# Optimization experiments

Measured on AMD Instinct MI355X. Metric: run time of the kernel, lower is better.

## Reference

```python
import jax, jax.numpy as jnp
import numpy as np

ND_WEIGHT = 1.0
NUM_CLASS = 1000
B, D = 16384, 2048


def setup_inputs() -> dict:
    key = jax.random.key(0)
    k1, k2, k3, k4 = jax.random.split(key, 4)
    s_emb = jax.random.normal(k1, (B, D), dtype=jnp.float32)
    t_emb = jax.random.normal(k2, (B, D), dtype=jnp.float32)
    T_EMB = jax.random.normal(k3, (NUM_CLASS, D), dtype=jnp.float32)
    labels = jax.random.randint(k4, (B,), 0, NUM_CLASS, dtype=jnp.int64)
    return {"s_emb": s_emb, "t_emb": t_emb, "T_EMB": T_EMB, "labels": labels}


def reference(s_emb, t_emb, T_EMB, labels):
    # Gather per-sample class centers: [B, D]
    centers = T_EMB[labels]
    # Unit-normalize each center (L2 along feature dim)
    e_c = centers / jnp.linalg.norm(centers, axis=-1, keepdims=True)
    # Per-sample max of student/teacher embedding norms: [B]
    s_norm = jnp.linalg.norm(s_emb, axis=-1)
    t_norm = jnp.linalg.norm(t_emb, axis=-1)
    max_norm = jnp.maximum(s_norm, t_norm)
    # 1 - <s, e_c> / max_norm, summed then averaged, scaled by nd_weight
    dots = jnp.sum(s_emb * e_c, axis=-1)
    loss_sum = jnp.sum(1.0 - dots / max_norm)
    return loss_sum * ND_WEIGHT / s_emb.shape[0]
```

## Files before the change

kernel.cpp:

```cpp
#include <hip/hip_runtime.h>


#define NROWS 16384
#define DDIM  2048
#define BLK   256

__global__ __launch_bounds__(BLK) void dnl_row_kernel(
    const float* __restrict__ s_emb,
    const float* __restrict__ t_emb,
    const float* __restrict__ T_EMB,
    const int*   __restrict__ labels,
    float*       __restrict__ partial)
{
    const int row = blockIdx.x;
    const int tid = threadIdx.x;
    const int label = labels[row];

    const float4* s4 = (const float4*)(s_emb + (size_t)row   * DDIM);
    const float4* t4 = (const float4*)(t_emb + (size_t)row   * DDIM);
    const float4* c4 = (const float4*)(T_EMB + (size_t)label * DDIM);

    float ss = 0.f, tt = 0.f, sc = 0.f, cc = 0.f;
    #pragma unroll
    for (int it = 0; it < 2; ++it) {
        const int k = tid + it * BLK;
        const float4 s = s4[k];
        const float4 t = t4[k];
        const float4 c = c4[k];
        ss += s.x*s.x + s.y*s.y + s.z*s.z + s.w*s.w;
        tt += t.x*t.x + t.y*t.y + t.z*t.z + t.w*t.w;
        sc += s.x*c.x + s.y*c.y + s.z*c.z + s.w*c.w;
        cc += c.x*c.x + c.y*c.y + c.z*c.z + c.w*c.w;
    }

    #pragma unroll
    for (int off = 32; off > 0; off >>= 1) {
        ss += __shfl_down(ss, off, 64);
        tt += __shfl_down(tt, off, 64);
        sc += __shfl_down(sc, off, 64);
        cc += __shfl_down(cc, off, 64);
    }

    __shared__ float red[4][4];
    const int wave = tid >> 6;
    const int lane = tid & 63;
    if (lane == 0) {
        red[wave][0] = ss; red[wave][1] = tt;
        red[wave][2] = sc; red[wave][3] = cc;
    }
    __syncthreads();

    if (tid == 0) {
        float SS = 0.f, TT = 0.f, SC = 0.f, CC = 0.f;
        #pragma unroll
        for (int w = 0; w < 4; ++w) {
            SS += red[w][0]; TT += red[w][1];
            SC += red[w][2]; CC += red[w][3];
        }
        const float max_norm = fmaxf(sqrtf(SS), sqrtf(TT));
        partial[row] = 1.0f - SC / (sqrtf(CC) * max_norm);
    }
}

__global__ __launch_bounds__(BLK) void dnl_row_kernel_atomic(
    const float* __restrict__ s_emb,
    const float* __restrict__ t_emb,
    const float* __restrict__ T_EMB,
    const int*   __restrict__ labels,
    float*       __restrict__ out)
{
    const int row = blockIdx.x;
    const int tid = threadIdx.x;
    const int label = labels[row];

    const float4* s4 = (const float4*)(s_emb + (size_t)row   * DDIM);
    const float4* t4 = (const float4*)(t_emb + (size_t)row   * DDIM);
    const float4* c4 = (const float4*)(T_EMB + (size_t)label * DDIM);

    float ss = 0.f, tt = 0.f, sc = 0.f, cc = 0.f;
    #pragma unroll
    for (int it = 0; it < 2; ++it) {
        const int k = tid + it * BLK;
        const float4 s = s4[k];
        const float4 t = t4[k];
        const float4 c = c4[k];
        ss += s.x*s.x + s.y*s.y + s.z*s.z + s.w*s.w;
        tt += t.x*t.x + t.y*t.y + t.z*t.z + t.w*t.w;
        sc += s.x*c.x + s.y*c.y + s.z*c.z + s.w*c.w;
        cc += c.x*c.x + c.y*c.y + c.z*c.z + c.w*c.w;
    }
    #pragma unroll
    for (int off = 32; off > 0; off >>= 1) {
        ss += __shfl_down(ss, off, 64);
        tt += __shfl_down(tt, off, 64);
        sc += __shfl_down(sc, off, 64);
        cc += __shfl_down(cc, off, 64);
    }
    __shared__ float red[4][4];
    const int wave = tid >> 6;
    const int lane = tid & 63;
    if (lane == 0) {
        red[wave][0] = ss; red[wave][1] = tt;
        red[wave][2] = sc; red[wave][3] = cc;
    }
    __syncthreads();
    if (tid == 0) {
        float SS = 0.f, TT = 0.f, SC = 0.f, CC = 0.f;
        #pragma unroll
        for (int w = 0; w < 4; ++w) {
            SS += red[w][0]; TT += red[w][1];
            SC += red[w][2]; CC += red[w][3];
        }
        const float max_norm = fmaxf(sqrtf(SS), sqrtf(TT));
        const float contrib = 1.0f - SC / (sqrtf(CC) * max_norm);
        atomicAdd(out, contrib * (1.0f / (float)NROWS));
    }
}

__global__ __launch_bounds__(BLK) void dnl_reduce_kernel(
    const float* __restrict__ partial,
    float*       __restrict__ out)
{
    const int tid = threadIdx.x;
    float sum = 0.f;
    for (int i = tid; i < NROWS; i += BLK) sum += partial[i];

    #pragma unroll
    for (int off = 32; off > 0; off >>= 1)
        sum += __shfl_down(sum, off, 64);

    __shared__ float red[4];
    if ((tid & 63) == 0) red[tid >> 6] = sum;
    __syncthreads();
    if (tid == 0)
        out[0] = (red[0] + red[1] + red[2] + red[3]) * (1.0f / (float)NROWS);
}

extern "C" void kernel_launch(void* const* d_in, const int* in_sizes, int n_in,
                              void* d_out, int out_size, void* d_ws, size_t ws_size,
                              hipStream_t stream) {
    const float* s_emb  = (const float*)d_in[0];
    const float* t_emb  = (const float*)d_in[1];
    const float* T_EMB  = (const float*)d_in[2];
    const int*   labels = (const int*)d_in[3];
    float* out = (float*)d_out;

    if (ws_size >= (size_t)NROWS * sizeof(float)) {
        float* partial = (float*)d_ws;
        dnl_row_kernel<<<NROWS, BLK, 0, stream>>>(s_emb, t_emb, T_EMB, labels, partial);
        dnl_reduce_kernel<<<1, BLK, 0, stream>>>(partial, out);
    } else {
        hipMemsetAsync(d_out, 0, sizeof(float), stream);
        dnl_row_kernel_atomic<<<NROWS, BLK, 0, stream>>>(s_emb, t_emb, T_EMB, labels, out);
    }
}
```

Measured before the change: 298.9 us.

## Process one row per wavefront in a persistent grid with per-wave accumulation

Replaces the one-block-per-row launch (16384 blocks) with a persistent grid of 1024 blocks where each 64-lane wavefront handles whole rows in a strided loop. Rows are reduced with xor shuffles only, so the shared-memory stage and __syncthreads go away, and each wave keeps a running sum plus a prefetched next label. The final reduction reads 4096 per-wave partials with float4 loads instead of 16384 per-row values. Each wave now issues 24 float4 loads per row, which gives more memory-level parallelism per wave. The cost is fewer total waves in flight to hide HBM latency.

```diff
diff --git a/kernel.cpp b/kernel.cpp
--- a/kernel.cpp
+++ b/kernel.cpp
@@ -1,139 +1,127 @@
 #include <hip/hip_runtime.h>
 
 
-#define NROWS 16384
-#define DDIM  2048
-#define BLK   256
+#define NROWS      16384
+#define DDIM       2048
+#define BLK        256
+#define GRID       1024
+#define NUM_WAVES  (GRID * (BLK / 64))
 
-__global__ __launch_bounds__(BLK) void dnl_row_kernel(
+__global__ __launch_bounds__(BLK) void dnl_main_kernel(
     const float* __restrict__ s_emb,
     const float* __restrict__ t_emb,
     const float* __restrict__ T_EMB,
     const int*   __restrict__ labels,
-    float*       __restrict__ partial)
+    float*       __restrict__ wavesum)
 {
-    const int row = blockIdx.x;
+    const int tid   = threadIdx.x;
+    const int lane  = tid & 63;
+    const int gwave = blockIdx.x * (BLK / 64) + (tid >> 6);
+
+    float acc = 0.f;
+    int next_label = labels[gwave];
+
+    for (int row = gwave; row < NROWS; row += NUM_WAVES) {
+        const int label = next_label;
+        const int nrow  = row + NUM_WAVES;
+        if (nrow < NROWS) next_label = labels[nrow];
+
+        const float4* s4 = (const float4*)(s_emb + (size_t)row   * DDIM);
+        const float4* t4 = (const float4*)(t_emb + (size_t)row   * DDIM);
+        const float4* c4 = (const float4*)(T_EMB + (size_t)label * DDIM);
+
+        float ss = 0.f, tt = 0.f, sc = 0.f, cc = 0.f;
+        #pragma unroll
+        for (int j = 0; j < 8; ++j) {
+            const int k = lane + j * 64;
+            const float4 s = s4[k];
+            const float4 t = t4[k];
+            const float4 c = c4[k];
+            ss += s.x*s.x + s.y*s.y + s.z*s.z + s.w*s.w;
+            tt += t.x*t.x + t.y*t.y + t.z*t.z + t.w*t.w;
+            sc += s.x*c.x + s.y*c.y + s.z*c.z + s.w*c.w;
+            cc += c.x*c.x + c.y*c.y + c.z*c.z + c.w*c.w;
+        }
+
+        #pragma unroll
+        for (int off = 32; off > 0; off >>= 1) {
+            ss += __shfl_xor(ss, off, 64);
+            tt += __shfl_xor(tt, off, 64);
+            sc += __shfl_xor(sc, off, 64);
+            cc += __shfl_xor(cc, off, 64);
+        }
+
+        const float max_norm = fmaxf(sqrtf(ss), sqrtf(tt));
+        acc += 1.0f - sc / (sqrtf(cc) * max_norm);
+    }
+
+    if (lane == 0) wavesum[gwave] = acc;
+}
+
+__global__ __launch_bounds__(BLK) void dnl_reduce_kernel(
+    const float* __restrict__ wavesum,
+    float*       __restrict__ out)
+{
     const int tid = threadIdx.x;
-    const int label = labels[row];
-
-    const float4* s4 = (const float4*)(s_emb + (size_t)row   * DDIM);
-    const float4* t4 = (const float4*)(t_emb + (size_t)row   * DDIM);
-    const float4* c4 = (const float4*)(T_EMB + (size_t)label * DDIM);
-
-    float ss = 0.f, tt = 0.f, sc = 0.f, cc = 0.f;
+    const float4* w4 = (const float4*)wavesum;
+    float sum = 0.f;
     #pragma unroll
-    for (int it = 0; it < 2; ++it) {
-        const int k = tid + it * BLK;
-        const float4 s = s4[k];
-        const float4 t = t4[k];
-        const float4 c = c4[k];
-        ss += s.x*s.x + s.y*s.y + s.z*s.z + s.w*s.w;
-        tt += t.x*t.x + t.y*t.y + t.z*t.z + t.w*t.w;
-        sc += s.x*c.x + s.y*c.y + s.z*c.z + s.w*c.w;
-        cc += c.x*c.x + c.y*c.y + c.z*c.z + c.w*c.w;
+    for (int j = 0; j < 4; ++j) {
+        const float4 v = w4[tid + j * BLK];
+        sum += v.x + v.y + v.z + v.w;
     }
 
     #pragma unroll
-    for (int off = 32; off > 0; off >>= 1) {
-        ss += __shfl_down(ss, off, 64);
-        tt += __shfl_down(tt, off, 64);
-        sc += __shfl_down(sc, off, 64);
-        cc += __shfl_down(cc, off, 64);
-    }
+    for (int off = 32; off > 0; off >>= 1)
+        sum += __shfl_xor(sum, off, 64);
 
-    __shared__ float red[4][4];
-    const int wave = tid >> 6;
-    const int lane = tid & 63;
-    if (lane == 0) {
-        red[wave][0] = ss; red[wave][1] = tt;
-        red[wave][2] = sc; red[wave][3] = cc;
-    }
+    __shared__ float red[4];
+    if ((tid & 63) == 0) red[tid >> 6] = sum;
     __syncthreads();
-
-    if (tid == 0) {
-        float SS = 0.f, TT = 0.f, SC = 0.f, CC = 0.f;
-        #pragma unroll
-        for (int w = 0; w < 4; ++w) {
-            SS += red[w][0]; TT += red[w][1];
-            SC += red[w][2]; CC += red[w][3];
-        }
-        const float max_norm = fmaxf(sqrtf(SS), sqrtf(TT));
-        partial[row] = 1.0f - SC / (sqrtf(CC) * max_norm);
-    }
+    if (tid == 0)
+        out[0] = (red[0] + red[1] + red[2] + red[3]) * (1.0f / (float)NROWS);
 }
 
-__global__ __launch_bounds__(BLK) void dnl_row_kernel_atomic(
+__global__ __launch_bounds__(BLK) void dnl_main_atomic_kernel(
     const float* __restrict__ s_emb,
     const float* __restrict__ t_emb,
     const float* __restrict__ T_EMB,
     const int*   __restrict__ labels,
     float*       __restrict__ out)
 {
-    const int row = blockIdx.x;
-    const int tid = threadIdx.x;
-    const int label = labels[row];
+    const int tid   = threadIdx.x;
+    const int lane  = tid & 63;
+    const int gwave = blockIdx.x * (BLK / 64) + (tid >> 6);
 
-    const float4* s4 = (const float4*)(s_emb + (size_t)row   * DDIM);
-    const float4* t4 = (const float4*)(t_emb + (size_t)row   * DDIM);
-    const float4* c4 = (const float4*)(T_EMB + (size_t)label * DDIM);
-
-    float ss = 0.f, tt = 0.f, sc = 0.f, cc = 0.f;
-    #pragma unroll
-    for (int it = 0; it < 2; ++it) {
-        const int k = tid + it * BLK;
-        const float4 s = s4[k];
-        const float4 t = t4[k];
-        const float4 c = c4[k];
-        ss += s.x*s.x + s.y*s.y + s.z*s.z + s.w*s.w;
-        tt += t.x*t.x + t.y*t.y + t.z*t.z + t.w*t.w;
-        sc += s.x*c.x + s.y*c.y + s.z*c.z + s.w*c.w;
-        cc += c.x*c.x + c.y*c.y + c.z*c.z + c.w*c.w;
+    float acc = 0.f;
+    for (int row = gwave; row < NROWS; row += NUM_WAVES) {
+        const int label = labels[row];
+        const float4* s4 = (const float4*)(s_emb + (size_t)row   * DDIM);
+        const float4* t4 = (const float4*)(t_emb + (size_t)row   * DDIM);
+        const float4* c4 = (const float4*)(T_EMB + (size_t)label * DDIM);
+        float ss = 0.f, tt = 0.f, sc = 0.f, cc = 0.f;
+        #pragma unroll
+        for (int j = 0; j < 8; ++j) {
+            const int k = lane + j * 64;
+            const float4 s = s4[k];
+            const float4 t = t4[k];
+            const float4 c = c4[k];
+            ss += s.x*s.x + s.y*s.y + s.z*s.z + s.w*s.w;
+            tt += t.x*t.x + t.y*t.y + t.z*t.z + t.w*t.w;
+            sc += s.x*c.x + s.y*c.y + s.z*c.z + s.w*c.w;
+            cc += c.x*c.x + c.y*c.y + c.z*c.z + c.w*c.w;
+        }
+        #pragma unroll
+        for (int off = 32; off > 0; off >>= 1) {
+            ss += __shfl_xor(ss, off, 64);
+            tt += __shfl_xor(tt, off, 64);
+            sc += __shfl_xor(sc, off, 64);
+            cc += __shfl_xor(cc, off, 64);
+        }
+        const float max_norm = fmaxf(sqrtf(ss), sqrtf(tt));
+        acc += 1.0f - sc / (sqrtf(cc) * max_norm);
     }
-    #pragma unroll
-    for (int off = 32; off > 0; off >>= 1) {
-        ss += __shfl_down(ss, off, 64);
-        tt += __shfl_down(tt, off, 64);
-        sc += __shfl_down(sc, off, 64);
-        cc += __shfl_down(cc, off, 64);
-    }
-    __shared__ float red[4][4];
-    const int wave = tid >> 6;
-    const int lane = tid & 63;
-    if (lane == 0) {
-        red[wave][0] = ss; red[wave][1] = tt;
-        red[wave][2] = sc; red[wave][3] = cc;
-    }
-    __syncthreads();
-    if (tid == 0) {
-        float SS = 0.f, TT = 0.f, SC = 0.f, CC = 0.f;
-        #pragma unroll
-        for (int w = 0; w < 4; ++w) {
-            SS += red[w][0]; TT += red[w][1];
-            SC += red[w][2]; CC += red[w][3];
-        }
-        const float max_norm = fmaxf(sqrtf(SS), sqrtf(TT));
-        const float contrib = 1.0f - SC / (sqrtf(CC) * max_norm);
-        atomicAdd(out, contrib * (1.0f / (float)NROWS));
-    }
-}
-
-__global__ __launch_bounds__(BLK) void dnl_reduce_kernel(
-    const float* __restrict__ partial,
-    float*       __restrict__ out)
-{
-    const int tid = threadIdx.x;
-    float sum = 0.f;
-    for (int i = tid; i < NROWS; i += BLK) sum += partial[i];
-
-    #pragma unroll
-    for (int off = 32; off > 0; off >>= 1)
-        sum += __shfl_down(sum, off, 64);
-
-    __shared__ float red[4];
-    if ((tid & 63) == 0) red[tid >> 6] = sum;
-    __syncthreads();
-    if (tid == 0)
-        out[0] = (red[0] + red[1] + red[2] + red[3]) * (1.0f / (float)NROWS);
+    if (lane == 0) atomicAdd(out, acc * (1.0f / (float)NROWS));
 }
 
 extern "C" void kernel_launch(void* const* d_in, const int* in_sizes, int n_in,
@@ -145,12 +133,12 @@
     const int*   labels = (const int*)d_in[3];
     float* out = (float*)d_out;
 
-    if (ws_size >= (size_t)NROWS * sizeof(float)) {
-        float* partial = (float*)d_ws;
-        dnl_row_kernel<<<NROWS, BLK, 0, stream>>>(s_emb, t_emb, T_EMB, labels, partial);
-        dnl_reduce_kernel<<<1, BLK, 0, stream>>>(partial, out);
+    if (ws_size >= (size_t)NUM_WAVES * sizeof(float)) {
+        float* wavesum = (float*)d_ws;
+        dnl_main_kernel<<<GRID, BLK, 0, stream>>>(s_emb, t_emb, T_EMB, labels, wavesum);
+        dnl_reduce_kernel<<<1, BLK, 0, stream>>>(wavesum, out);
     } else {
         hipMemsetAsync(d_out, 0, sizeof(float), stream);
-        dnl_row_kernel_atomic<<<NROWS, BLK, 0, stream>>>(s_emb, t_emb, T_EMB, labels, out);
+        dnl_main_atomic_kernel<<<GRID, BLK, 0, stream>>>(s_emb, t_emb, T_EMB, labels, out);
     }
 }
```

Measured after the change: 287.9 us. -3.7%, faster.
